# Performance work log

Measured on AMD Instinct MI355X. Metric: run time of the kernel, lower is better.

The kernel has to match this reference:

```python
import jax, jax.numpy as jnp
import numpy as np

N_NODES = 100000
N_EDGES = 1600000
DIM = 128
NUM_HEADS = 8
HEAD_DIM = DIM // NUM_HEADS


def setup_inputs() -> dict:
    key = jax.random.key(0)
    k_x, k_src, k_dst, k_wqkv, k_bqkv, k_wout, k_bout = jax.random.split(key, 7)
    x = jax.random.normal(k_x, (N_NODES, DIM), dtype=jnp.float32)
    src = jax.random.randint(k_src, (N_EDGES,), 0, N_NODES, dtype=jnp.int32)
    dst = jax.random.randint(k_dst, (N_EDGES,), 0, N_NODES, dtype=jnp.int32)
    s = 1.0 / np.sqrt(DIM)
    Wqkv = jax.random.uniform(k_wqkv, (DIM, 3 * DIM), jnp.float32, -s, s)
    bqkv = jax.random.uniform(k_bqkv, (3 * DIM,), jnp.float32, -s, s)
    Wout = jax.random.uniform(k_wout, (DIM, DIM), jnp.float32, -s, s)
    bout = jax.random.uniform(k_bout, (DIM,), jnp.float32, -s, s)
    return {"x": x, "Wqkv": Wqkv, "bqkv": bqkv, "Wout": Wout, "bout": bout,
            "src": src, "dst": dst}


def reference(x, Wqkv, bqkv, Wout, bout, src, dst):
    n = x.shape[0]
    scale = 1.0 / np.sqrt(HEAD_DIM)
    # QKV projection -> [N, H, 3*hd], split exactly like torch .split on last dim
    qkv = (x @ Wqkv + bqkv).reshape(n, NUM_HEADS, 3 * HEAD_DIM)
    q = qkv[..., :HEAD_DIM]                       # queries  [N, H, hd]
    k = qkv[..., HEAD_DIM:2 * HEAD_DIM]           # keys     [N, H, hd]
    v = qkv[..., 2 * HEAD_DIM:]                   # values   [N, H, hd]
    # u_dot_v: per edge (u=src, v=dst): dot(keys[u], queries[v]) per head
    scores = jnp.einsum('ehd,ehd->eh', k[src], q[dst]) * scale  # [E, H]
    # edge_softmax over incoming edges of each dst node
    m = jax.ops.segment_max(scores, dst, num_segments=n)        # [N, H]
    p = jnp.exp(scores - m[dst])                                # [E, H]
    denom = jax.ops.segment_sum(p, dst, num_segments=n)         # [N, H]
    probs = p / denom[dst]                                      # [E, H]
    # u_mul_e_sum: scatter-sum of values[src] * probs into dst
    msgs = v[src] * probs[:, :, None]                            # [E, H, hd]
    agg = jax.ops.segment_sum(msgs, dst, num_segments=n)         # [N, H, hd]
    out = agg.reshape(n, DIM) @ Wout + bout
    return out
```

## Files before the change

kernel.cpp:

```cpp
#include <hip/hip_runtime.h>
#include <cstdint>
#include <cstddef>

#define N_DIM 128
#define QKV_DIM 384
#define NUM_HEADS 8
#define HEAD_DIM 16
#define SCAN_B 256
#define SCAN_V 4
#define SCAN_TILE (SCAN_B * SCAN_V)

typedef unsigned int uint;
typedef unsigned short ushort;
typedef __attribute__((ext_vector_type(8))) short short8;
typedef __attribute__((ext_vector_type(4))) float f32x4;

__device__ __forceinline__ ushort f2bf(float f) {
    uint u = __float_as_uint(f);
    uint r = u + 0x7fffu + ((u >> 16) & 1u);
    return (ushort)(r >> 16);
}
__device__ __forceinline__ float bf_lo(uint u) { return __uint_as_float(u << 16); }
__device__ __forceinline__ float bf_hi(uint u) { return __uint_as_float(u & 0xffff0000u); }

__global__ void pack_w_kernel(const float* __restrict__ Wq, const float* __restrict__ Wo,
                              ushort* __restrict__ WpQ, ushort* __restrict__ WpO) {
    int idx = blockIdx.x * blockDim.x + threadIdx.x;
    const float* W;
    ushort* Wp;
    int N;
    if (idx < 128 * QKV_DIM) {
        W = Wq; Wp = WpQ; N = QKV_DIM;
    } else {
        idx -= 128 * QKV_DIM;
        if (idx >= 128 * N_DIM) return;
        W = Wo; Wp = WpO; N = N_DIM;
    }
    int j = idx & 7;
    int l = (idx >> 3) & 63;
    int fs = idx >> 9;
    int T = fs >> 2, s = fs & 3;
    int k = s * 32 + (l >> 4) * 8 + j;
    int c = T * 16 + (l & 15);
    Wp[idx] = f2bf(W[k * N + c]);
}

__global__ __launch_bounds__(256) void qkv_gemm(const float* __restrict__ x,
                                                const ushort* __restrict__ Wp,
                                                const float* __restrict__ bqkv,
                                                float* __restrict__ qtab,
                                                ushort* __restrict__ kvb, int n) {
    int w = threadIdx.x >> 6, lane = threadIdx.x & 63;
    int node0 = blockIdx.x * 64 + w * 16;
    int m = lane & 15, quad = lane >> 4;
    int arow = node0 + m; if (arow >= n) arow = n - 1;
    const float* xr = x + (size_t)arow * N_DIM;
    short8 A[4];
    #pragma unroll
    for (int s = 0; s < 4; ++s) {
        float4 f0 = *(const float4*)(xr + s * 32 + quad * 8);
        float4 f1 = *(const float4*)(xr + s * 32 + quad * 8 + 4);
        uint u0 = (uint)f2bf(f0.x) | ((uint)f2bf(f0.y) << 16);
        uint u1 = (uint)f2bf(f0.z) | ((uint)f2bf(f0.w) << 16);
        uint u2 = (uint)f2bf(f1.x) | ((uint)f2bf(f1.y) << 16);
        uint u3 = (uint)f2bf(f1.z) | ((uint)f2bf(f1.w) << 16);
        uint4 u = make_uint4(u0, u1, u2, u3);
        A[s] = *(short8*)&u;
    }
    for (int T = 0; T < 24; ++T) {
        f32x4 acc = {0.f, 0.f, 0.f, 0.f};
        const ushort* bp = Wp + ((size_t)(T * 4) * 64 + lane) * 8;
        #pragma unroll
        for (int s = 0; s < 4; ++s) {
            uint4 u = *(const uint4*)(bp + s * 512);
            short8 B = *(short8*)&u;
            acc = __builtin_amdgcn_mfma_f32_16x16x32_bf16(A[s], B, acc, 0, 0, 0);
        }
        int c = T * 16 + m;
        int hq = T / 3, wv = T % 3;
        float bb = bqkv[c];
        #pragma unroll
        for (int r = 0; r < 4; ++r) {
            int nd = node0 + quad * 4 + r;
            if (nd < n) {
                float v = acc[r] + bb;
                if (wv == 0) {
                    qtab[(size_t)nd * N_DIM + hq * 16 + m] = v;
                } else {
                    kvb[(size_t)nd * 256 + hq * 32 + (wv - 1) * 16 + m] = f2bf(v);
                }
            }
        }
    }
}

__global__ __launch_bounds__(256) void out_gemm(const uint* __restrict__ aggb,
                                                const ushort* __restrict__ Wp,
                                                const float* __restrict__ bout,
                                                float* __restrict__ out, int n) {
    int w = threadIdx.x >> 6, lane = threadIdx.x & 63;
    int node0 = blockIdx.x * 64 + w * 16;
    int m = lane & 15, quad = lane >> 4;
    int arow = node0 + m; if (arow >= n) arow = n - 1;
    const uint* ar = aggb + (size_t)arow * 64;
    short8 A[4];
    #pragma unroll
    for (int s = 0; s < 4; ++s) {
        uint4 u = *(const uint4*)(ar + s * 16 + quad * 4);
        A[s] = *(short8*)&u;
    }
    for (int T = 0; T < 8; ++T) {
        f32x4 acc = {0.f, 0.f, 0.f, 0.f};
        const ushort* bp = Wp + ((size_t)(T * 4) * 64 + lane) * 8;
        #pragma unroll
        for (int s = 0; s < 4; ++s) {
            uint4 u = *(const uint4*)(bp + s * 512);
            short8 B = *(short8*)&u;
            acc = __builtin_amdgcn_mfma_f32_16x16x32_bf16(A[s], B, acc, 0, 0, 0);
        }
        int c = T * 16 + m;
        float bb = bout[c];
        #pragma unroll
        for (int r = 0; r < 4; ++r) {
            int nd = node0 + quad * 4 + r;
            if (nd < n) out[(size_t)nd * N_DIM + c] = acc[r] + bb;
        }
    }
}

__global__ void hist_kernel(const int* __restrict__ dst, int* __restrict__ counts, int nE) {
    int e = blockIdx.x * blockDim.x + threadIdx.x;
    if (e < nE) atomicAdd(&counts[dst[e]], 1);
}

__global__ void scan1_kernel(const int* __restrict__ counts, int* __restrict__ offs,
                             int* __restrict__ partials, int n) {
    __shared__ int ts[SCAN_B];
    int t = threadIdx.x;
    int base = blockIdx.x * SCAN_TILE + t * SCAN_V;
    int v[SCAN_V];
    int s = 0;
    #pragma unroll
    for (int i = 0; i < SCAN_V; ++i) { v[i] = (base + i < n) ? counts[base + i] : 0; s += v[i]; }
    ts[t] = s;
    __syncthreads();
    for (int off = 1; off < SCAN_B; off <<= 1) {
        int x = (t >= off) ? ts[t - off] : 0;
        __syncthreads();
        ts[t] += x;
        __syncthreads();
    }
    int run = (t > 0) ? ts[t - 1] : 0;
    if (t == SCAN_B - 1) partials[blockIdx.x] = ts[SCAN_B - 1];
    #pragma unroll
    for (int i = 0; i < SCAN_V; ++i) { if (base + i < n) offs[base + i] = run; run += v[i]; }
}

__global__ void scan2_kernel(int* __restrict__ partials, int P) {
    __shared__ int ps[1024];
    int t = threadIdx.x;
    ps[t] = (t < P) ? partials[t] : 0;
    __syncthreads();
    for (int off = 1; off < 1024; off <<= 1) {
        int x = (t >= off) ? ps[t - off] : 0;
        __syncthreads();
        ps[t] += x;
        __syncthreads();
    }
    if (t < P) partials[t] = (t > 0) ? ps[t - 1] : 0;
}

__global__ void scan3_kernel(int* __restrict__ offs, const int* __restrict__ partials,
                             int* __restrict__ cursor, int n, int nE) {
    int i = blockIdx.x * blockDim.x + threadIdx.x;
    if (i < n) {
        int o = offs[i] + partials[i / SCAN_TILE];
        offs[i] = o;
        cursor[i] = o;
    }
    if (i == 0) offs[n] = nE;
}

__global__ __launch_bounds__(256) void scatter_src_shard(const int* __restrict__ src,
                                                         const int* __restrict__ dst,
                                                         int* __restrict__ cursor,
                                                         int* __restrict__ esrc,
                                                         int nE, int shardSize) {
    int shard = blockIdx.x & 7;
    int sub   = blockIdx.x >> 3;
    int nsub  = gridDim.x >> 3;
    int lo = shard * shardSize;
    int hi = lo + shardSize;
    int stride = nsub * blockDim.x;
    for (int e = sub * blockDim.x + threadIdx.x; e < nE; e += stride) {
        int d = dst[e];
        if (d >= lo && d < hi) {
            int pos = atomicAdd(&cursor[d], 1);
            esrc[pos] = src[e];
        }
    }
}

__global__ void attn_kernel(const float* __restrict__ qtab, const uint* __restrict__ kvu,
                            const int* __restrict__ esrc, const int* __restrict__ offs,
                            ushort* __restrict__ aggb, int n) {
    int node = blockIdx.x;
    int t = threadIdx.x;
    __shared__ float qs[16][8];
    __shared__ uint  so[16];
    __shared__ float pp[16][8];
    __shared__ float lw[2][8];
    int h  = t >> 4, dd = t & 15;
    int h2 = t & 7,  el = t >> 3;
    {
        float qv = qtab[(size_t)node * N_DIM + t];
        qs[dd][h] = qv;
    }
    int start = offs[node];
    int deg = offs[node + 1] - start;
    float lsum = 0.f, acc = 0.f;
    int voff = h * 16 + 8 + (dd >> 1);
    bool hi = (dd & 1);
    __syncthreads();

    for (int c0 = 0; c0 < deg; c0 += 16) {
        int rem = deg - c0;
        int cn = rem < 16 ? rem : 16;
        if (t < 16) so[t] = (t < cn) ? ((uint)esrc[start + c0 + t] << 9) : 0u;
        __syncthreads();
        float pv = 0.f;
        if (el < cn) {
            const uint* kr = (const uint*)((const char*)kvu + so[el]) + h2 * 16;
            uint4 A = *((const uint4*)kr);
            uint4 B = *((const uint4*)(kr + 4));
            float dot = 0.f;
            dot = fmaf(bf_lo(A.x), qs[0][h2],  dot); dot = fmaf(bf_hi(A.x), qs[1][h2],  dot);
            dot = fmaf(bf_lo(A.y), qs[2][h2],  dot); dot = fmaf(bf_hi(A.y), qs[3][h2],  dot);
            dot = fmaf(bf_lo(A.z), qs[4][h2],  dot); dot = fmaf(bf_hi(A.z), qs[5][h2],  dot);
            dot = fmaf(bf_lo(A.w), qs[6][h2],  dot); dot = fmaf(bf_hi(A.w), qs[7][h2],  dot);
            dot = fmaf(bf_lo(B.x), qs[8][h2],  dot); dot = fmaf(bf_hi(B.x), qs[9][h2],  dot);
            dot = fmaf(bf_lo(B.y), qs[10][h2], dot); dot = fmaf(bf_hi(B.y), qs[11][h2], dot);
            dot = fmaf(bf_lo(B.z), qs[12][h2], dot); dot = fmaf(bf_hi(B.z), qs[13][h2], dot);
            dot = fmaf(bf_lo(B.w), qs[14][h2], dot); dot = fmaf(bf_hi(B.w), qs[15][h2], dot);
            pv = __expf(dot * 0.25f);
        }
        pp[el][h2] = pv;
        lsum += pv;
        __syncthreads();
        float vacc = 0.f;
        if (cn == 16) {
            uint vv[16];
            #pragma unroll
            for (int i = 0; i < 16; ++i) {
                uint off = (uint)__builtin_amdgcn_readfirstlane((int)so[i]);
                vv[i] = *((const uint*)((const char*)kvu + off) + voff);
            }
            #pragma unroll
            for (int i = 0; i < 16; ++i) {
                float p = pp[i][h];
                float v = hi ? bf_hi(vv[i]) : bf_lo(vv[i]);
                vacc = fmaf(p, v, vacc);
            }
        } else {
            for (int i = 0; i < cn; ++i) {
                uint off = (uint)__builtin_amdgcn_readfirstlane((int)so[i]);
                float p = pp[i][h];
                uint u = *((const uint*)((const char*)kvu + off) + voff);
                float v = hi ? bf_hi(u) : bf_lo(u);
                vacc = fmaf(p, v, vacc);
            }
        }
        acc += vacc;
        __syncthreads();
    }
    lsum += __shfl_xor(lsum, 8, 64);
    lsum += __shfl_xor(lsum, 16, 64);
    lsum += __shfl_xor(lsum, 32, 64);
    if ((t & 63) < 8) lw[t >> 6][t & 7] = lsum;
    __syncthreads();
    float l = lw[0][h] + lw[1][h];
    aggb[(size_t)node * N_DIM + t] = f2bf((l > 0.f) ? acc / l : 0.f);
}

extern "C" void kernel_launch(void* const* d_in, const int* in_sizes, int n_in,
                              void* d_out, int out_size, void* d_ws, size_t ws_size,
                              hipStream_t stream) {
    const float* x    = (const float*)d_in[0];
    const float* Wqkv = (const float*)d_in[1];
    const float* bqkv = (const float*)d_in[2];
    const float* Wout = (const float*)d_in[3];
    const float* bout = (const float*)d_in[4];
    const int*   src  = (const int*)d_in[5];
    const int*   dst  = (const int*)d_in[6];
    float* out = (float*)d_out;

    const int n  = in_sizes[0] / N_DIM;
    const int nE = in_sizes[5];

    uint* ws = (uint*)d_ws;
    float*  qtab   = (float*)ws;
    uint*   kvu    = ws + (size_t)n * 128;
    uint*   aggb   = kvu + (size_t)n * 128;
    ushort* WpQ    = (ushort*)(aggb + (size_t)n * 64);
    ushort* WpO    = WpQ + 128 * QKV_DIM;
    int*    counts = (int*)(WpO + 128 * N_DIM);
    int*    offs   = counts + n;
    int*    cursor = offs + n + 1;
    int*    partials = cursor + n;
    int*    esrc   = partials + 1024;

    hipMemsetAsync(counts, 0, (size_t)n * sizeof(int), stream);

    pack_w_kernel<<<(128 * (QKV_DIM + N_DIM) + 255) / 256, 256, 0, stream>>>(Wqkv, Wout, WpQ, WpO);

    qkv_gemm<<<(n + 63) / 64, 256, 0, stream>>>(x, WpQ, bqkv, qtab, (ushort*)kvu, n);

    hist_kernel<<<(nE + 255) / 256, 256, 0, stream>>>(dst, counts, nE);
    int P = (n + SCAN_TILE - 1) / SCAN_TILE;
    scan1_kernel<<<P, SCAN_B, 0, stream>>>(counts, offs, partials, n);
    scan2_kernel<<<1, 1024, 0, stream>>>(partials, P);
    scan3_kernel<<<(n + 255) / 256, 256, 0, stream>>>(offs, partials, cursor, n, nE);

    int shardSize = (n + 7) / 8;
    scatter_src_shard<<<8 * 128, 256, 0, stream>>>(src, dst, cursor, esrc, nE, shardSize);

    attn_kernel<<<n, 128, 0, stream>>>(qtab, kvu, esrc, offs, (ushort*)aggb, n);

    out_gemm<<<(n + 63) / 64, 256, 0, stream>>>(aggb, WpO, bout, out, n);
}
```

Before: 470.2 us.

## Split V aggregation across waves by edge, each lane handling two bf16 values

The V-weighted aggregation now splits each 16-edge chunk across the two waves, 8 edges per wave. Each lane loads one packed uint of two bf16 values and accumulates both into separate registers. The old scheme had every thread walk all 16 edges for a single element. The per-wave partial sums are combined through shared memory at the end. This halves per-thread loads and FMAs in the aggregation loop and widens the offset reads, at the cost of an extra shared-memory reduction.

```diff
diff --git a/kernel.cpp b/kernel.cpp
--- a/kernel.cpp
+++ b/kernel.cpp
@@ -210,17 +210,20 @@
     __shared__ uint  so[16];
     __shared__ float pp[16][8];
     __shared__ float lw[2][8];
-    int h  = t >> 4, dd = t & 15;
+    __shared__ float accs[2][8][8][2];
     int h2 = t & 7,  el = t >> 3;
+    int wv = t >> 6, l  = t & 63;
+    int hB = l >> 3, jB = l & 7;
+    int hA = t >> 4, dd = t & 15;
     {
         float qv = qtab[(size_t)node * N_DIM + t];
-        qs[dd][h] = qv;
+        qs[dd][hA] = qv;
     }
     int start = offs[node];
     int deg = offs[node + 1] - start;
-    float lsum = 0.f, acc = 0.f;
-    int voff = h * 16 + 8 + (dd >> 1);
-    bool hi = (dd & 1);
+    float lsum = 0.f;
+    float accx = 0.f, accy = 0.f;
+    uint voffb = (uint)hB * 64u + 32u + (uint)jB * 4u;
     __syncthreads();
 
     for (int c0 = 0; c0 < deg; c0 += 16) {
@@ -230,7 +233,7 @@
         __syncthreads();
         float pv = 0.f;
         if (el < cn) {
-            const uint* kr = (const uint*)((const char*)kvu + so[el]) + h2 * 16;
+            const uint* kr = (const uint*)((const char*)kvu + so[el] + (uint)h2 * 64u);
             uint4 A = *((const uint4*)kr);
             uint4 B = *((const uint4*)(kr + 4));
             float dot = 0.f;
@@ -247,39 +250,56 @@
         pp[el][h2] = pv;
         lsum += pv;
         __syncthreads();
-        float vacc = 0.f;
         if (cn == 16) {
-            uint vv[16];
+            uint4 s0 = *(const uint4*)&so[wv * 8];
+            uint4 s1 = *(const uint4*)&so[wv * 8 + 4];
+            uint o0 = s0.x, o1 = s0.y, o2 = s0.z, o3 = s0.w;
+            uint o4 = s1.x, o5 = s1.y, o6 = s1.z, o7 = s1.w;
+            uint u0 = *(const uint*)((const char*)kvu + (o0 + voffb));
+            uint u1 = *(const uint*)((const char*)kvu + (o1 + voffb));
+            uint u2 = *(const uint*)((const char*)kvu + (o2 + voffb));
+            uint u3 = *(const uint*)((const char*)kvu + (o3 + voffb));
+            uint u4 = *(const uint*)((const char*)kvu + (o4 + voffb));
+            uint u5 = *(const uint*)((const char*)kvu + (o5 + voffb));
+            uint u6 = *(const uint*)((const char*)kvu + (o6 + voffb));
+            uint u7 = *(const uint*)((const char*)kvu + (o7 + voffb));
+            int eb = wv * 8;
+            float p0 = pp[eb + 0][hB], p1 = pp[eb + 1][hB];
+            float p2 = pp[eb + 2][hB], p3 = pp[eb + 3][hB];
+            float p4 = pp[eb + 4][hB], p5 = pp[eb + 5][hB];
+            float p6 = pp[eb + 6][hB], p7 = pp[eb + 7][hB];
+            accx = fmaf(p0, bf_lo(u0), accx); accy = fmaf(p0, bf_hi(u0), accy);
+            accx = fmaf(p1, bf_lo(u1), accx); accy = fmaf(p1, bf_hi(u1), accy);
+            accx = fmaf(p2, bf_lo(u2), accx); accy = fmaf(p2, bf_hi(u2), accy);
+            accx = fmaf(p3, bf_lo(u3), accx); accy = fmaf(p3, bf_hi(u3), accy);
+            accx = fmaf(p4, bf_lo(u4), accx); accy = fmaf(p4, bf_hi(u4), accy);
+            accx = fmaf(p5, bf_lo(u5), accx); accy = fmaf(p5, bf_hi(u5), accy);
+            accx = fmaf(p6, bf_lo(u6), accx); accy = fmaf(p6, bf_hi(u6), accy);
+            accx = fmaf(p7, bf_lo(u7), accx); accy = fmaf(p7, bf_hi(u7), accy);
+        } else {
             #pragma unroll
-            for (int i = 0; i < 16; ++i) {
-                uint off = (uint)__builtin_amdgcn_readfirstlane((int)so[i]);
-                vv[i] = *((const uint*)((const char*)kvu + off) + voff);
+            for (int i = 0; i < 8; ++i) {
+                int idx = wv * 8 + i;
+                if (idx < cn) {
+                    uint u = *(const uint*)((const char*)kvu + (so[idx] + voffb));
+                    float p = pp[idx][hB];
+                    accx = fmaf(p, bf_lo(u), accx);
+                    accy = fmaf(p, bf_hi(u), accy);
+                }
             }
-            #pragma unroll
-            for (int i = 0; i < 16; ++i) {
-                float p = pp[i][h];
-                float v = hi ? bf_hi(vv[i]) : bf_lo(vv[i]);
-                vacc = fmaf(p, v, vacc);
-            }
-        } else {
-            for (int i = 0; i < cn; ++i) {
-                uint off = (uint)__builtin_amdgcn_readfirstlane((int)so[i]);
-                float p = pp[i][h];
-                uint u = *((const uint*)((const char*)kvu + off) + voff);
-                float v = hi ? bf_hi(u) : bf_lo(u);
-                vacc = fmaf(p, v, vacc);
-            }
-        }
-        acc += vacc;
-        __syncthreads();
-    }
+        }
+        __syncthreads();
+    }
+    accs[wv][hB][jB][0] = accx;
+    accs[wv][hB][jB][1] = accy;
     lsum += __shfl_xor(lsum, 8, 64);
     lsum += __shfl_xor(lsum, 16, 64);
     lsum += __shfl_xor(lsum, 32, 64);
-    if ((t & 63) < 8) lw[t >> 6][t & 7] = lsum;
+    if (l < 8) lw[wv][l] = lsum;
     __syncthreads();
-    float l = lw[0][h] + lw[1][h];
-    aggb[(size_t)node * N_DIM + t] = f2bf((l > 0.f) ? acc / l : 0.f);
+    float L = lw[0][hA] + lw[1][hA];
+    float val = accs[0][hA][dd >> 1][dd & 1] + accs[1][hA][dd >> 1][dd & 1];
+    aggb[(size_t)node * N_DIM + t] = f2bf((L > 0.f) ? val / L : 0.f);
 }
 
 extern "C" void kernel_launch(void* const* d_in, const int* in_sizes, int n_in,
```

After: 452.2 us. 3.8% less time.

## Map one wavefront per node in attention kernel, replacing LDS sync with shuffles

Applied to the files above, without the earlier changes.

The attention kernel now processes four nodes per 256-thread block, one 64-lane wavefront per node, instead of one node per 128-thread block. Edge indices and softmax weights are exchanged with wavefront shuffles rather than shared memory, which removes the block-wide barriers inside the edge loop. Each lane accumulates two output features and writes them as a packed pair of bf16 values. Edges are processed in chunks of 8 instead of 16, so there are fewer loads in flight per iteration and more loop trips for high-degree nodes.

```diff
diff --git a/kernel.cpp b/kernel.cpp
--- a/kernel.cpp
+++ b/kernel.cpp
@@ -201,85 +201,73 @@
     }
 }
 
-__global__ void attn_kernel(const float* __restrict__ qtab, const uint* __restrict__ kvu,
+__global__ __launch_bounds__(256) void attn_kernel(const float* __restrict__ qtab,
+                            const uint* __restrict__ kvu,
                             const int* __restrict__ esrc, const int* __restrict__ offs,
                             ushort* __restrict__ aggb, int n) {
-    int node = blockIdx.x;
-    int t = threadIdx.x;
-    __shared__ float qs[16][8];
-    __shared__ uint  so[16];
-    __shared__ float pp[16][8];
-    __shared__ float lw[2][8];
-    int h  = t >> 4, dd = t & 15;
-    int h2 = t & 7,  el = t >> 3;
-    {
-        float qv = qtab[(size_t)node * N_DIM + t];
-        qs[dd][h] = qv;
-    }
-    int start = offs[node];
-    int deg = offs[node + 1] - start;
-    float lsum = 0.f, acc = 0.f;
-    int voff = h * 16 + 8 + (dd >> 1);
-    bool hi = (dd & 1);
+    int wv = threadIdx.x >> 6;
+    int l  = threadIdx.x & 63;
+    int node = blockIdx.x * 4 + wv;
+    __shared__ float qs[4][16][8];
+    int el = l >> 3, h2 = l & 7;
+    int hB = l >> 3, jB = l & 7;
+    bool active = (node < n);
+    int start = 0, deg = 0;
+    if (active) {
+        float2 qv = *(const float2*)(qtab + (size_t)node * N_DIM + l * 2);
+        int e = l * 2;
+        qs[wv][e & 15][e >> 4] = qv.x;
+        qs[wv][(e + 1) & 15][e >> 4] = qv.y;
+        start = offs[node];
+        deg = offs[node + 1] - start;
+    }
     __syncthreads();
-
-    for (int c0 = 0; c0 < deg; c0 += 16) {
+    float qr[16];
+    #pragma unroll
+    for (int d = 0; d < 16; ++d) qr[d] = qs[wv][d][h2];
+
+    float lsum = 0.f, accx = 0.f, accy = 0.f;
+    uint voffb = (uint)hB * 64u + 32u + (uint)jB * 4u;
+
+    for (int c0 = 0; c0 < deg; c0 += 8) {
         int rem = deg - c0;
-        int cn = rem < 16 ? rem : 16;
-        if (t < 16) so[t] = (t < cn) ? ((uint)esrc[start + c0 + t] << 9) : 0u;
-        __syncthreads();
+        int cn = rem < 8 ? rem : 8;
+        uint sov = 0u;
+        if (l < cn) sov = (uint)esrc[start + c0 + l] << 9;
+        uint soA = __shfl(sov, el);
         float pv = 0.f;
         if (el < cn) {
-            const uint* kr = (const uint*)((const char*)kvu + so[el]) + h2 * 16;
+            const uint* kr = (const uint*)((const char*)kvu + soA + (uint)h2 * 64u);
             uint4 A = *((const uint4*)kr);
             uint4 B = *((const uint4*)(kr + 4));
             float dot = 0.f;
-            dot = fmaf(bf_lo(A.x), qs[0][h2],  dot); dot = fmaf(bf_hi(A.x), qs[1][h2],  dot);
-            dot = fmaf(bf_lo(A.y), qs[2][h2],  dot); dot = fmaf(bf_hi(A.y), qs[3][h2],  dot);
-            dot = fmaf(bf_lo(A.z), qs[4][h2],  dot); dot = fmaf(bf_hi(A.z), qs[5][h2],  dot);
-            dot = fmaf(bf_lo(A.w), qs[6][h2],  dot); dot = fmaf(bf_hi(A.w), qs[7][h2],  dot);
-            dot = fmaf(bf_lo(B.x), qs[8][h2],  dot); dot = fmaf(bf_hi(B.x), qs[9][h2],  dot);
-            dot = fmaf(bf_lo(B.y), qs[10][h2], dot); dot = fmaf(bf_hi(B.y), qs[11][h2], dot);
-            dot = fmaf(bf_lo(B.z), qs[12][h2], dot); dot = fmaf(bf_hi(B.z), qs[13][h2], dot);
-            dot = fmaf(bf_lo(B.w), qs[14][h2], dot); dot = fmaf(bf_hi(B.w), qs[15][h2], dot);
+            dot = fmaf(bf_lo(A.x), qr[0],  dot); dot = fmaf(bf_hi(A.x), qr[1],  dot);
+            dot = fmaf(bf_lo(A.y), qr[2],  dot); dot = fmaf(bf_hi(A.y), qr[3],  dot);
+            dot = fmaf(bf_lo(A.z), qr[4],  dot); dot = fmaf(bf_hi(A.z), qr[5],  dot);
+            dot = fmaf(bf_lo(A.w), qr[6],  dot); dot = fmaf(bf_hi(A.w), qr[7],  dot);
+            dot = fmaf(bf_lo(B.x), qr[8],  dot); dot = fmaf(bf_hi(B.x), qr[9],  dot);
+            dot = fmaf(bf_lo(B.y), qr[10], dot); dot = fmaf(bf_hi(B.y), qr[11], dot);
+            dot = fmaf(bf_lo(B.z), qr[12], dot); dot = fmaf(bf_hi(B.z), qr[13], dot);
+            dot = fmaf(bf_lo(B.w), qr[14], dot); dot = fmaf(bf_hi(B.w), qr[15], dot);
             pv = __expf(dot * 0.25f);
         }
-        pp[el][h2] = pv;
         lsum += pv;
-        __syncthreads();
-        float vacc = 0.f;
-        if (cn == 16) {
-            uint vv[16];
-            #pragma unroll
-            for (int i = 0; i < 16; ++i) {
-                uint off = (uint)__builtin_amdgcn_readfirstlane((int)so[i]);
-                vv[i] = *((const uint*)((const char*)kvu + off) + voff);
-            }
-            #pragma unroll
-            for (int i = 0; i < 16; ++i) {
-                float p = pp[i][h];
-                float v = hi ? bf_hi(vv[i]) : bf_lo(vv[i]);
-                vacc = fmaf(p, v, vacc);
-            }
-        } else {
-            for (int i = 0; i < cn; ++i) {
-                uint off = (uint)__builtin_amdgcn_readfirstlane((int)so[i]);
-                float p = pp[i][h];
-                uint u = *((const uint*)((const char*)kvu + off) + voff);
-                float v = hi ? bf_hi(u) : bf_lo(u);
-                vacc = fmaf(p, v, vacc);
-            }
-        }
-        acc += vacc;
-        __syncthreads();
-    }
-    lsum += __shfl_xor(lsum, 8, 64);
-    lsum += __shfl_xor(lsum, 16, 64);
-    lsum += __shfl_xor(lsum, 32, 64);
-    if ((t & 63) < 8) lw[t >> 6][t & 7] = lsum;
-    __syncthreads();
-    float l = lw[0][h] + lw[1][h];
-    aggb[(size_t)node * N_DIM + t] = f2bf((l > 0.f) ? acc / l : 0.f);
+        #pragma unroll
+        for (int i = 0; i < 8; ++i) {
+            uint so_i = __shfl(sov, i);
+            float p_i = __shfl(pv, i * 8 + hB);
+            uint u = *(const uint*)((const char*)kvu + (so_i + voffb));
+            accx = fmaf(p_i, bf_lo(u), accx);
+            accy = fmaf(p_i, bf_hi(u), accy);
+        }
+    }
+    lsum += __shfl_xor(lsum, 8);
+    lsum += __shfl_xor(lsum, 16);
+    lsum += __shfl_xor(lsum, 32);
+    float L = __shfl(lsum, hB);
+    float rL = (L > 0.f) ? 1.f / L : 0.f;
+    uint pack = (uint)f2bf(accx * rL) | ((uint)f2bf(accy * rL) << 16);
+    if (active) ((uint*)aggb)[(size_t)node * 64 + l] = pack;
 }
 
 extern "C" void kernel_launch(void* const* d_in, const int* in_sizes, int n_in,
@@ -324,7 +312,7 @@
     int shardSize = (n + 7) / 8;
     scatter_src_shard<<<8 * 128, 256, 0, stream>>>(src, dst, cursor, esrc, nE, shardSize);
 
-    attn_kernel<<<n, 128, 0, stream>>>(qtab, kvu, esrc, offs, (ushort*)aggb, n);
+    attn_kernel<<<(n + 3) / 4, 256, 0, stream>>>(qtab, kvu, esrc, offs, (ushort*)aggb, n);
 
     out_gemm<<<(n + 63) / 64, 256, 0, stream>>>(aggb, WpO, bout, out, n);
 }
```

After: 463.2 us. Within noise of the previous version (-1.5%).

## Fuse histogram into QKV GEMM and stage GEMM outputs through LDS for coalesced stores

Applied to the files above, without the earlier changes.

The dst-degree histogram atomics move into the QKV GEMM kernel as a grid-stride loop, which removes one kernel launch. The GEMM epilogue now writes Q and KV tiles into shared memory per wave, then stores them to global memory as 16-byte vectors instead of scattered scalar stores. The attention kernel's V-gather addressing changes from readfirstlane-based offsets to plain byte-offset arithmetic. The cost is about 24KB of LDS per block, which may limit occupancy, and atomics now running inside the GEMM.

```diff
diff --git a/kernel.cpp b/kernel.cpp
--- a/kernel.cpp
+++ b/kernel.cpp
@@ -49,7 +49,17 @@
                                                 const ushort* __restrict__ Wp,
                                                 const float* __restrict__ bqkv,
                                                 float* __restrict__ qtab,
-                                                ushort* __restrict__ kvb, int n) {
+                                                ushort* __restrict__ kvb,
+                                                const int* __restrict__ dst,
+                                                int* __restrict__ counts,
+                                                int n, int nE) {
+    {
+        int stride = gridDim.x * blockDim.x;
+        for (int e = blockIdx.x * blockDim.x + threadIdx.x; e < nE; e += stride)
+            atomicAdd(&counts[dst[e]], 1);
+    }
+    __shared__ float  lq[4][16][64];
+    __shared__ ushort lkv[4][16][128];
     int w = threadIdx.x >> 6, lane = threadIdx.x & 63;
     int node0 = blockIdx.x * 64 + w * 16;
     int m = lane & 15, quad = lane >> 4;
@@ -67,29 +77,43 @@
         uint4 u = make_uint4(u0, u1, u2, u3);
         A[s] = *(short8*)&u;
     }
-    for (int T = 0; T < 24; ++T) {
-        f32x4 acc = {0.f, 0.f, 0.f, 0.f};
-        const ushort* bp = Wp + ((size_t)(T * 4) * 64 + lane) * 8;
+    for (int half = 0; half < 2; ++half) {
+        for (int T12 = 0; T12 < 12; ++T12) {
+            int T = half * 12 + T12;
+            f32x4 acc = {0.f, 0.f, 0.f, 0.f};
+            const ushort* bp = Wp + ((size_t)(T * 4) * 64 + lane) * 8;
+            #pragma unroll
+            for (int s = 0; s < 4; ++s) {
+                uint4 u = *(const uint4*)(bp + s * 512);
+                short8 B = *(short8*)&u;
+                acc = __builtin_amdgcn_mfma_f32_16x16x32_bf16(A[s], B, acc, 0, 0, 0);
+            }
+            int c = T * 16 + m;
+            int hq = T / 3, wvv = T % 3;
+            int hl = hq - half * 4;
+            float bb = bqkv[c];
+            #pragma unroll
+            for (int r = 0; r < 4; ++r) {
+                int nd16 = quad * 4 + r;
+                float v = acc[r] + bb;
+                if (wvv == 0) lq[w][nd16][hl * 16 + m] = v;
+                else          lkv[w][nd16][hl * 32 + (wvv - 1) * 16 + m] = f2bf(v);
+            }
+        }
         #pragma unroll
-        for (int s = 0; s < 4; ++s) {
-            uint4 u = *(const uint4*)(bp + s * 512);
-            short8 B = *(short8*)&u;
-            acc = __builtin_amdgcn_mfma_f32_16x16x32_bf16(A[s], B, acc, 0, 0, 0);
-        }
-        int c = T * 16 + m;
-        int hq = T / 3, wv = T % 3;
-        float bb = bqkv[c];
-        #pragma unroll
-        for (int r = 0; r < 4; ++r) {
-            int nd = node0 + quad * 4 + r;
-            if (nd < n) {
-                float v = acc[r] + bb;
-                if (wv == 0) {
-                    qtab[(size_t)nd * N_DIM + hq * 16 + m] = v;
-                } else {
-                    kvb[(size_t)nd * 256 + hq * 32 + (wv - 1) * 16 + m] = f2bf(v);
-                }
-            }
+        for (int rr = 0; rr < 4; ++rr) {
+            int of = rr * 256 + lane * 4;
+            int ndq = of >> 6, colq = of & 63;
+            float4 qv = *(const float4*)&lq[w][ndq][colq];
+            int gq = node0 + ndq;
+            if (gq < n)
+                *(float4*)(qtab + (size_t)gq * N_DIM + half * 64 + colq) = qv;
+            int ou = rr * 512 + lane * 8;
+            int ndk = ou >> 7, elk = ou & 127;
+            uint4 kvv = *(const uint4*)&lkv[w][ndk][elk];
+            int gk = node0 + ndk;
+            if (gk < n)
+                *(uint4*)(kvb + (size_t)gk * 256 + half * 128 + elk) = kvv;
         }
     }
 }
@@ -126,11 +150,6 @@
             if (nd < n) out[(size_t)nd * N_DIM + c] = acc[r] + bb;
         }
     }
-}
-
-__global__ void hist_kernel(const int* __restrict__ dst, int* __restrict__ counts, int nE) {
-    int e = blockIdx.x * blockDim.x + threadIdx.x;
-    if (e < nE) atomicAdd(&counts[dst[e]], 1);
 }
 
 __global__ void scan1_kernel(const int* __restrict__ counts, int* __restrict__ offs,
@@ -219,7 +238,7 @@
     int start = offs[node];
     int deg = offs[node + 1] - start;
     float lsum = 0.f, acc = 0.f;
-    int voff = h * 16 + 8 + (dd >> 1);
+    uint voffb = (uint)h * 64u + 32u + (uint)(dd >> 1) * 4u;
     bool hi = (dd & 1);
     __syncthreads();
 
@@ -230,7 +249,7 @@
         __syncthreads();
         float pv = 0.f;
         if (el < cn) {
-            const uint* kr = (const uint*)((const char*)kvu + so[el]) + h2 * 16;
+            const uint* kr = (const uint*)((const char*)kvu + so[el] + (uint)h2 * 64u);
             uint4 A = *((const uint4*)kr);
             uint4 B = *((const uint4*)(kr + 4));
             float dot = 0.f;
@@ -251,10 +270,8 @@
         if (cn == 16) {
             uint vv[16];
             #pragma unroll
-            for (int i = 0; i < 16; ++i) {
-                uint off = (uint)__builtin_amdgcn_readfirstlane((int)so[i]);
-                vv[i] = *((const uint*)((const char*)kvu + off) + voff);
-            }
+            for (int i = 0; i < 16; ++i)
+                vv[i] = *(const uint*)((const char*)kvu + (so[i] + voffb));
             #pragma unroll
             for (int i = 0; i < 16; ++i) {
                 float p = pp[i][h];
@@ -263,9 +280,8 @@
             }
         } else {
             for (int i = 0; i < cn; ++i) {
-                uint off = (uint)__builtin_amdgcn_readfirstlane((int)so[i]);
+                uint u = *(const uint*)((const char*)kvu + (so[i] + voffb));
                 float p = pp[i][h];
-                uint u = *((const uint*)((const char*)kvu + off) + voff);
                 float v = hi ? bf_hi(u) : bf_lo(u);
                 vacc = fmaf(p, v, vacc);
             }
@@ -278,8 +294,8 @@
     lsum += __shfl_xor(lsum, 32, 64);
     if ((t & 63) < 8) lw[t >> 6][t & 7] = lsum;
     __syncthreads();
-    float l = lw[0][h] + lw[1][h];
-    aggb[(size_t)node * N_DIM + t] = f2bf((l > 0.f) ? acc / l : 0.f);
+    float L = lw[0][h] + lw[1][h];
+    aggb[(size_t)node * N_DIM + t] = f2bf((L > 0.f) ? acc / L : 0.f);
 }
 
 extern "C" void kernel_launch(void* const* d_in, const int* in_sizes, int n_in,
@@ -313,9 +329,9 @@
 
     pack_w_kernel<<<(128 * (QKV_DIM + N_DIM) + 255) / 256, 256, 0, stream>>>(Wqkv, Wout, WpQ, WpO);
 
-    qkv_gemm<<<(n + 63) / 64, 256, 0, stream>>>(x, WpQ, bqkv, qtab, (ushort*)kvu, n);
-
-    hist_kernel<<<(nE + 255) / 256, 256, 0, stream>>>(dst, counts, nE);
+    qkv_gemm<<<(n + 63) / 64, 256, 0, stream>>>(x, WpQ, bqkv, qtab, (ushort*)kvu,
+                                                dst, counts, n, nE);
+
     int P = (n + SCAN_TILE - 1) / SCAN_TILE;
     scan1_kernel<<<P, SCAN_B, 0, stream>>>(counts, offs, partials, n);
     scan2_kernel<<<1, 1024, 0, stream>>>(partials, P);
```

Result: faster. 432.1 us (-8.1%).
